# Optimization experiments

Hardware: AMD Instinct MI355X
Metric: run time of the kernel (lower is better)

The kernel has to match this reference:

```python
import jax, jax.numpy as jnp
import numpy as np

N = 1024
X_DIM = 256
Y_DIM = 256
HIDDEN = 256


def setup_inputs() -> dict:
    key = jax.random.key(0)
    ks = jax.random.split(key, 6)
    lim1 = 1.0 / np.sqrt(X_DIM + Y_DIM)
    lim2 = 1.0 / np.sqrt(HIDDEN)
    return {
        "x_samples": jax.random.normal(ks[0], (N, X_DIM), jnp.float32),
        "y_samples": jax.random.normal(ks[1], (N, Y_DIM), jnp.float32),
        # F_func params: Linear(x_dim+y_dim, hidden) -> ReLU -> Linear(hidden, 1)
        "W1": jax.random.uniform(ks[2], (X_DIM + Y_DIM, HIDDEN), jnp.float32, -lim1, lim1),
        "b1": jax.random.uniform(ks[3], (HIDDEN,), jnp.float32, -lim1, lim1),
        "W2": jax.random.uniform(ks[4], (HIDDEN, 1), jnp.float32, -lim2, lim2),
        "b2": jax.random.uniform(ks[5], (1,), jnp.float32, -lim2, lim2),
    }


def reference(x_samples, y_samples, W1, b1, W2, b2):
    n = y_samples.shape[0]
    # Diagonal (joint) term: F([x_i, y_i])
    t0 = jnp.maximum(jnp.concatenate([x_samples, y_samples], axis=-1) @ W1 + b1, 0.0) @ W2 + b2  # [N,1]
    # Pairwise term: decompose first Linear into x- and y-projections, broadcast-sum.
    px = x_samples @ W1[:X_DIM]   # [N, H]
    py = y_samples @ W1[X_DIM:]   # [N, H]
    # torch layout: row axis = y tile, col axis = x tile -> h[i, j] = relu(py_i + px_j + b1)
    h = jnp.maximum(py[:, None, :] + px[None, :, :] + b1, 0.0)          # [N, N, H]
    t1 = jnp.einsum("yxh,ho->yx", h, W2) + b2[0] - 1.0                   # [N, N]
    # logsumexp over dim=1 (x axis), then exp-mean
    lse = jax.nn.logsumexp(t1, axis=1) - jnp.log(jnp.float32(n))         # [N]
    lower_bound = t0.mean() - jnp.exp(lse).mean()
    return lower_bound
```

## Files before the change

### kernel.cpp

```cpp
#include <hip/hip_runtime.h>

#define NS 1024
#define KD 256
#define H  256
#define NBLK 256

__global__ __launch_bounds__(256) void proj_kernel(
    const float* __restrict__ X, const float* __restrict__ Y,
    const float* __restrict__ W1, const float* __restrict__ b1,
    float* __restrict__ PX, float* __restrict__ PYB, int* __restrict__ counter)
{
    if (blockIdx.x == 0 && blockIdx.y == 0 && blockIdx.z == 0 && threadIdx.x == 0)
        *counter = 0;

    const int z = blockIdx.z;
    const float* __restrict__ A = z ? Y : X;
    const float* __restrict__ W = W1 + (z ? KD * H : 0);
    float* __restrict__ OUT = z ? PYB : PX;

    __shared__ float xs[KD][34];

    const int tid = threadIdx.x;
    const int tx = tid & 15;
    const int ty = tid >> 4;
    const int i0 = blockIdx.y * 32, h0 = blockIdx.x * 64;

    {
        const int ii = tid & 31, q = tid >> 5;
        #pragma unroll
        for (int u = 0; u < 8; ++u) {
            const int k = u * 32 + q * 4;
            float4 v = *(const float4*)&A[(i0 + ii) * KD + k];
            xs[k + 0][ii] = v.x; xs[k + 1][ii] = v.y;
            xs[k + 2][ii] = v.z; xs[k + 3][ii] = v.w;
        }
    }
    __syncthreads();

    float acc[2][4] = {};
    const float* __restrict__ wp = &W[h0 + tx * 4];

    #pragma unroll 8
    for (int k = 0; k < KD; ++k) {
        float4 w4 = *(const float4*)&wp[k * H];
        const float x0 = xs[k][ty * 2 + 0];
        const float x1 = xs[k][ty * 2 + 1];
        acc[0][0] = fmaf(x0, w4.x, acc[0][0]);
        acc[0][1] = fmaf(x0, w4.y, acc[0][1]);
        acc[0][2] = fmaf(x0, w4.z, acc[0][2]);
        acc[0][3] = fmaf(x0, w4.w, acc[0][3]);
        acc[1][0] = fmaf(x1, w4.x, acc[1][0]);
        acc[1][1] = fmaf(x1, w4.y, acc[1][1]);
        acc[1][2] = fmaf(x1, w4.z, acc[1][2]);
        acc[1][3] = fmaf(x1, w4.w, acc[1][3]);
    }

    float bv[4] = {0.f, 0.f, 0.f, 0.f};
    if (z) *(float4*)bv = *(const float4*)&b1[h0 + tx * 4];
    #pragma unroll
    for (int r = 0; r < 2; ++r) {
        float o[4];
        #pragma unroll
        for (int c = 0; c < 4; ++c) o[c] = acc[r][c] + bv[c];
        *(float4*)&OUT[(i0 + ty * 2 + r) * H + h0 + tx * 4] = *(float4*)o;
    }
}

#define PXPAD 132
#define PYPAD 34

__global__ __launch_bounds__(256) void pair_kernel(
    const float* __restrict__ PX, const float* __restrict__ PYB,
    const float* __restrict__ W2, const float* __restrict__ b2,
    float* __restrict__ eparts, float* __restrict__ dparts,
    int* __restrict__ counter, float* __restrict__ out)
{
    __shared__ float pxt[2][64][PXPAD];
    __shared__ float pyt[2][64][PYPAD];
    __shared__ float red_e[256], red_d[256];
    __shared__ double sde[256], sdd[256];
    __shared__ int lastflag;

    const int tid = threadIdx.x;
    const int tx = tid & 15;
    const int ty = tid >> 4;
    const int j0 = blockIdx.x * 128, i0 = blockIdx.y * 32;

    const int su = tid & 7;
    const int sjb = tid >> 3;
    const int sii = tid & 31;
    const int sq = tid >> 5;

    float acc[2][8] = {};

#define STAGE(T, B)                                                                  \
    {                                                                                \
        const int hb = (T) * 64;                                                     \
        _Pragma("unroll")                                                            \
        for (int t = 0; t < 4; ++t) {                                                \
            _Pragma("unroll")                                                        \
            for (int s = 0; s < 2; ++s) {                                            \
                const int j = sjb + 32 * t;                                          \
                const int hh = (su + 8 * s) * 4;                                     \
                float4 v = *(const float4*)&PX[(j0 + j) * H + hb + hh];              \
                pxt[B][hh + 0][j] = v.x; pxt[B][hh + 1][j] = v.y;                    \
                pxt[B][hh + 2][j] = v.z; pxt[B][hh + 3][j] = v.w;                    \
            }                                                                        \
        }                                                                            \
        _Pragma("unroll")                                                            \
        for (int s = 0; s < 2; ++s) {                                                \
            const int hh = sq * 8 + s * 4;                                           \
            float4 v = *(const float4*)&PYB[(i0 + sii) * H + hb + hh];               \
            pyt[B][hh + 0][sii] = v.x; pyt[B][hh + 1][sii] = v.y;                    \
            pyt[B][hh + 2][sii] = v.z; pyt[B][hh + 3][sii] = v.w;                    \
        }                                                                            \
    }

    STAGE(0, 0);
    __syncthreads();

    for (int t = 0; t < 4; ++t) {
        const int cur = t & 1;
        if (t < 3) {
            if ((t & 1) == 0) STAGE(t + 1, 1)
            else              STAGE(t + 1, 0)
        }
        const int hb = t * 64;
        #pragma unroll 4
        for (int hh = 0; hh < 64; ++hh) {
            const float w = W2[hb + hh];
            const float py0 = pyt[cur][hh][ty * 2 + 0];
            const float py1 = pyt[cur][hh][ty * 2 + 1];
            float a4[4], b4[4];
            *(float4*)a4 = *(const float4*)&pxt[cur][hh][tx * 4];
            *(float4*)b4 = *(const float4*)&pxt[cur][hh][64 + tx * 4];
            #pragma unroll
            for (int c = 0; c < 4; ++c) {
                acc[0][c]     = fmaf(fmaxf(py0 + a4[c], 0.f), w, acc[0][c]);
                acc[1][c]     = fmaf(fmaxf(py1 + a4[c], 0.f), w, acc[1][c]);
                acc[0][4 + c] = fmaf(fmaxf(py0 + b4[c], 0.f), w, acc[0][4 + c]);
                acc[1][4 + c] = fmaf(fmaxf(py1 + b4[c], 0.f), w, acc[1][4 + c]);
            }
        }
        __syncthreads();
    }

    const float c0 = b2[0] - 1.0f;
    float esum = 0.f, dsum = 0.f;
    #pragma unroll
    for (int r = 0; r < 2; ++r) {
        const int irow = i0 + ty * 2 + r;
        #pragma unroll
        for (int g = 0; g < 2; ++g)
            #pragma unroll
            for (int c = 0; c < 4; ++c) {
                const float t1 = acc[r][g * 4 + c] + c0;
                esum += expf(t1);
                if (irow == j0 + g * 64 + tx * 4 + c) dsum += t1 + 1.0f;
            }
    }

    red_e[tid] = esum;
    red_d[tid] = dsum;
    __syncthreads();
    for (int s = 128; s > 0; s >>= 1) {
        if (tid < s) {
            red_e[tid] += red_e[tid + s];
            red_d[tid] += red_d[tid + s];
        }
        __syncthreads();
    }

    const int bid = blockIdx.y * gridDim.x + blockIdx.x;
    if (tid == 0) {
        __hip_atomic_store(&eparts[bid], red_e[0], __ATOMIC_RELAXED, __HIP_MEMORY_SCOPE_AGENT);
        __hip_atomic_store(&dparts[bid], red_d[0], __ATOMIC_RELAXED, __HIP_MEMORY_SCOPE_AGENT);
        __threadfence();
        const int prev = __hip_atomic_fetch_add(counter, 1, __ATOMIC_ACQ_REL, __HIP_MEMORY_SCOPE_AGENT);
        lastflag = (prev == NBLK - 1);
    }
    __syncthreads();

    if (lastflag) {
        __threadfence();
        sde[tid] = (double)__hip_atomic_load(&eparts[tid], __ATOMIC_RELAXED, __HIP_MEMORY_SCOPE_AGENT);
        sdd[tid] = (double)__hip_atomic_load(&dparts[tid], __ATOMIC_RELAXED, __HIP_MEMORY_SCOPE_AGENT);
        __syncthreads();
        for (int s = 128; s > 0; s >>= 1) {
            if (tid < s) { sde[tid] += sde[tid + s]; sdd[tid] += sdd[tid + s]; }
            __syncthreads();
        }
        if (tid == 0)
            out[0] = (float)(sdd[0] / (double)NS - sde[0] / ((double)NS * (double)NS));
    }
}

extern "C" void kernel_launch(void* const* d_in, const int* in_sizes, int n_in,
                              void* d_out, int out_size, void* d_ws, size_t ws_size,
                              hipStream_t stream)
{
    const float* X  = (const float*)d_in[0];
    const float* Y  = (const float*)d_in[1];
    const float* W1 = (const float*)d_in[2];
    const float* b1 = (const float*)d_in[3];
    const float* W2 = (const float*)d_in[4];
    const float* b2 = (const float*)d_in[5];
    float* out = (float*)d_out;

    float* PX     = (float*)d_ws;
    float* PYB    = PX + NS * H;
    float* eparts = PYB + NS * H;
    float* dparts = eparts + 256;
    int*   counter = (int*)(dparts + 256);

    proj_kernel<<<dim3(H / 64, NS / 32, 2), 256, 0, stream>>>(X, Y, W1, b1, PX, PYB, counter);
    pair_kernel<<<dim3(8, 32), 256, 0, stream>>>(PX, PYB, W2, b2, eparts, dparts, counter, out);
}
```

Baseline: 122.0 us.

## Fold W2 into projections and use relu(a)=(a+|a|)/2 with sign-partitioned hidden units

The projection kernel now scales each hidden unit by its W2 weight and permutes units so that positive-weight units come first. The pair kernel computes w*relu(s) as 0.5*(s + |s|) for positive w and 0.5*(s - |s|) for negative w. The linear parts factor into per-row and per-column sums, so the inner loop becomes an add plus an abs-accumulate with no multiply. The pair kernel also switches to square 64x64 tiles with a 4x4 register block, swizzled shared memory, and register-staged prefetch. The risks are the per-step sign branch and extra fp32 rounding from the reassociation.

New measurement: 125.5 us. 1.03x slower.

```diff
diff --git a/kernel.cpp b/kernel.cpp
--- a/kernel.cpp
+++ b/kernel.cpp
@@ -5,24 +5,47 @@
 #define H  256
 #define NBLK 256
 
+__device__ __forceinline__ int ldsw(int hh, int j) {
+    return (hh << 6) + ((j + ((hh >> 2) << 2)) & 63);
+}
+
 __global__ __launch_bounds__(256) void proj_kernel(
     const float* __restrict__ X, const float* __restrict__ Y,
     const float* __restrict__ W1, const float* __restrict__ b1,
-    float* __restrict__ PX, float* __restrict__ PYB, int* __restrict__ counter)
+    const float* __restrict__ W2,
+    float* __restrict__ PXW, float* __restrict__ PYW, int* __restrict__ counter)
 {
     if (blockIdx.x == 0 && blockIdx.y == 0 && blockIdx.z == 0 && threadIdx.x == 0)
         *counter = 0;
 
+    __shared__ float xs[KD][34];
+    __shared__ int dsts[H];
+    __shared__ int woff[4];
+
+    const int tid = threadIdx.x;
+
+    {
+        const float w = W2[tid];
+        const bool pos = (w >= 0.0f);
+        const unsigned long long m = __ballot(pos);
+        const int lane = tid & 63, wv = tid >> 6;
+        const int below = __popcll(m & ((1ull << lane) - 1ull));
+        if (lane == 0) woff[wv] = __popcll(m);
+        __syncthreads();
+        const int npos = woff[0] + woff[1] + woff[2] + woff[3];
+        int posbase = 0;
+        #pragma unroll
+        for (int q = 0; q < 4; ++q) if (q < wv) posbase += woff[q];
+        const int negbase = npos + (wv * 64 - posbase);
+        dsts[tid] = pos ? (posbase + below) : (negbase + (lane - below));
+    }
+
     const int z = blockIdx.z;
     const float* __restrict__ A = z ? Y : X;
     const float* __restrict__ W = W1 + (z ? KD * H : 0);
-    float* __restrict__ OUT = z ? PYB : PX;
-
-    __shared__ float xs[KD][34];
-
-    const int tid = threadIdx.x;
-    const int tx = tid & 15;
-    const int ty = tid >> 4;
+    float* __restrict__ OUT = z ? PYW : PXW;
+
+    const int tx = tid & 15, ty = tid >> 4;
     const int i0 = blockIdx.y * 32, h0 = blockIdx.x * 64;
 
     {
@@ -39,7 +62,6 @@
 
     float acc[2][4] = {};
     const float* __restrict__ wp = &W[h0 + tx * 4];
-
     #pragma unroll 8
     for (int k = 0; k < KD; ++k) {
         float4 w4 = *(const float4*)&wp[k * H];
@@ -57,108 +79,151 @@
 
     float bv[4] = {0.f, 0.f, 0.f, 0.f};
     if (z) *(float4*)bv = *(const float4*)&b1[h0 + tx * 4];
+    float wv4[4];
+    *(float4*)wv4 = *(const float4*)&W2[h0 + tx * 4];
+    int d4[4];
+    *(int4*)d4 = *(const int4*)&dsts[h0 + tx * 4];
+
     #pragma unroll
     for (int r = 0; r < 2; ++r) {
-        float o[4];
-        #pragma unroll
-        for (int c = 0; c < 4; ++c) o[c] = acc[r][c] + bv[c];
-        *(float4*)&OUT[(i0 + ty * 2 + r) * H + h0 + tx * 4] = *(float4*)o;
-    }
-}
-
-#define PXPAD 132
-#define PYPAD 34
+        const int row = i0 + ty * 2 + r;
+        #pragma unroll
+        for (int c = 0; c < 4; ++c)
+            OUT[row * H + d4[c]] = (acc[r][c] + bv[c]) * wv4[c];
+    }
+}
 
 __global__ __launch_bounds__(256) void pair_kernel(
-    const float* __restrict__ PX, const float* __restrict__ PYB,
+    const float* __restrict__ PXW, const float* __restrict__ PYW,
     const float* __restrict__ W2, const float* __restrict__ b2,
     float* __restrict__ eparts, float* __restrict__ dparts,
     int* __restrict__ counter, float* __restrict__ out)
 {
-    __shared__ float pxt[2][64][PXPAD];
-    __shared__ float pyt[2][64][PYPAD];
+    __shared__ float pxt[2][64 * 64];
+    __shared__ float pyt[2][64 * 64];
+    __shared__ float fpx[4 * 64], fpy[4 * 64];
     __shared__ float red_e[256], red_d[256];
     __shared__ double sde[256], sdd[256];
+    __shared__ int wcnt[4];
     __shared__ int lastflag;
 
     const int tid = threadIdx.x;
-    const int tx = tid & 15;
-    const int ty = tid >> 4;
-    const int j0 = blockIdx.x * 128, i0 = blockIdx.y * 32;
-
-    const int su = tid & 7;
-    const int sjb = tid >> 3;
-    const int sii = tid & 31;
-    const int sq = tid >> 5;
-
-    float acc[2][8] = {};
-
-#define STAGE(T, B)                                                                  \
-    {                                                                                \
-        const int hb = (T) * 64;                                                     \
-        _Pragma("unroll")                                                            \
-        for (int t = 0; t < 4; ++t) {                                                \
-            _Pragma("unroll")                                                        \
-            for (int s = 0; s < 2; ++s) {                                            \
-                const int j = sjb + 32 * t;                                          \
-                const int hh = (su + 8 * s) * 4;                                     \
-                float4 v = *(const float4*)&PX[(j0 + j) * H + hb + hh];              \
-                pxt[B][hh + 0][j] = v.x; pxt[B][hh + 1][j] = v.y;                    \
-                pxt[B][hh + 2][j] = v.z; pxt[B][hh + 3][j] = v.w;                    \
-            }                                                                        \
-        }                                                                            \
-        _Pragma("unroll")                                                            \
-        for (int s = 0; s < 2; ++s) {                                                \
-            const int hh = sq * 8 + s * 4;                                           \
-            float4 v = *(const float4*)&PYB[(i0 + sii) * H + hb + hh];               \
-            pyt[B][hh + 0][sii] = v.x; pyt[B][hh + 1][sii] = v.y;                    \
-            pyt[B][hh + 2][sii] = v.z; pyt[B][hh + 3][sii] = v.w;                    \
-        }                                                                            \
-    }
-
-    STAGE(0, 0);
-    __syncthreads();
-
-    for (int t = 0; t < 4; ++t) {
-        const int cur = t & 1;
-        if (t < 3) {
-            if ((t & 1) == 0) STAGE(t + 1, 1)
-            else              STAGE(t + 1, 0)
-        }
-        const int hb = t * 64;
-        #pragma unroll 4
-        for (int hh = 0; hh < 64; ++hh) {
-            const float w = W2[hb + hh];
-            const float py0 = pyt[cur][hh][ty * 2 + 0];
-            const float py1 = pyt[cur][hh][ty * 2 + 1];
-            float a4[4], b4[4];
-            *(float4*)a4 = *(const float4*)&pxt[cur][hh][tx * 4];
-            *(float4*)b4 = *(const float4*)&pxt[cur][hh][64 + tx * 4];
+    const int tx = tid & 15, ty = tid >> 4;
+    const int j0 = blockIdx.x * 64, i0 = blockIdx.y * 64;
+
+    {
+        const float w = W2[tid];
+        const unsigned long long m = __ballot(w >= 0.0f);
+        if ((tid & 63) == 0) wcnt[tid >> 6] = __popcll(m);
+    }
+
+    const int su = tid & 15, jb = tid >> 4;
+    float4 sx[4], sy[4];
+
+#define GLOAD(T)                                                              \
+    {                                                                         \
+        const int hb = (T) * 64;                                              \
+        _Pragma("unroll")                                                     \
+        for (int t = 0; t < 4; ++t) {                                         \
+            sx[t] = *(const float4*)&PXW[(j0 + jb + 16 * t) * H + hb + su * 4];\
+            sy[t] = *(const float4*)&PYW[(i0 + jb + 16 * t) * H + hb + su * 4];\
+        }                                                                     \
+    }
+
+#define SWRITE(B)                                                             \
+    {                                                                         \
+        _Pragma("unroll")                                                     \
+        for (int t = 0; t < 4; ++t) {                                         \
+            const int j = jb + 16 * t;                                        \
+            pxt[B][ldsw(su * 4 + 0, j)] = sx[t].x;                            \
+            pxt[B][ldsw(su * 4 + 1, j)] = sx[t].y;                            \
+            pxt[B][ldsw(su * 4 + 2, j)] = sx[t].z;                            \
+            pxt[B][ldsw(su * 4 + 3, j)] = sx[t].w;                            \
+            pyt[B][ldsw(su * 4 + 0, j)] = sy[t].x;                            \
+            pyt[B][ldsw(su * 4 + 1, j)] = sy[t].y;                            \
+            pyt[B][ldsw(su * 4 + 2, j)] = sy[t].z;                            \
+            pyt[B][ldsw(su * 4 + 3, j)] = sy[t].w;                            \
+        }                                                                     \
+    }
+
+    GLOAD(0);
+    SWRITE(0);
+    __syncthreads();
+    const int Npos = wcnt[0] + wcnt[1] + wcnt[2] + wcnt[3];
+
+    float accP[4][4] = {}, accN[4][4] = {};
+    float fx = 0.f, fy = 0.f;
+    const int fj = tid & 63, fq = tid >> 6;
+
+    for (int T = 0; T < 4; ++T) {
+        const int cur = T & 1;
+        if (T < 3) GLOAD(T + 1);
+        const int hb = T * 64;
+
+        #pragma unroll
+        for (int g = 0; g < 16; ++g) {
+            const int rot = (g << 2);
+            const float* bx = &pxt[cur][(g << 8) + ((tx * 4 + rot) & 63)];
+            const float* by = &pyt[cur][(g << 8) + ((ty * 4 + rot) & 63)];
             #pragma unroll
-            for (int c = 0; c < 4; ++c) {
-                acc[0][c]     = fmaf(fmaxf(py0 + a4[c], 0.f), w, acc[0][c]);
-                acc[1][c]     = fmaf(fmaxf(py1 + a4[c], 0.f), w, acc[1][c]);
-                acc[0][4 + c] = fmaf(fmaxf(py0 + b4[c], 0.f), w, acc[0][4 + c]);
-                acc[1][4 + c] = fmaf(fmaxf(py1 + b4[c], 0.f), w, acc[1][4 + c]);
+            for (int k = 0; k < 4; ++k) {
+                float px4[4], py4[4];
+                *(float4*)px4 = *(const float4*)&bx[k * 64];
+                *(float4*)py4 = *(const float4*)&by[k * 64];
+                if (hb + (g << 2) + k < Npos) {
+                    #pragma unroll
+                    for (int r = 0; r < 4; ++r)
+                        #pragma unroll
+                        for (int c = 0; c < 4; ++c)
+                            accP[r][c] += fabsf(py4[r] + px4[c]);
+                } else {
+                    #pragma unroll
+                    for (int r = 0; r < 4; ++r)
+                        #pragma unroll
+                        for (int c = 0; c < 4; ++c)
+                            accN[r][c] += fabsf(py4[r] + px4[c]);
+                }
             }
         }
-        __syncthreads();
-    }
+
+        #pragma unroll
+        for (int s = 0; s < 16; ++s) {
+            const int hh = fq * 16 + s;
+            fx += pxt[cur][ldsw(hh, fj)];
+            fy += pyt[cur][ldsw(hh, fj)];
+        }
+
+        if (T < 3) SWRITE((T + 1) & 1);
+        __syncthreads();
+    }
+
+    fpx[fq * 64 + fj] = fx;
+    fpy[fq * 64 + fj] = fy;
+    __syncthreads();
 
     const float c0 = b2[0] - 1.0f;
+    float ffe[4], gge[4];
+    #pragma unroll
+    for (int c = 0; c < 4; ++c) {
+        const int j = tx * 4 + c;
+        ffe[c] = 0.5f * (fpx[j] + fpx[64 + j] + fpx[128 + j] + fpx[192 + j]);
+    }
+    #pragma unroll
+    for (int r = 0; r < 4; ++r) {
+        const int i = ty * 4 + r;
+        gge[r] = 0.5f * (fpy[i] + fpy[64 + i] + fpy[128 + i] + fpy[192 + i]) + c0;
+    }
+
     float esum = 0.f, dsum = 0.f;
     #pragma unroll
-    for (int r = 0; r < 2; ++r) {
-        const int irow = i0 + ty * 2 + r;
-        #pragma unroll
-        for (int g = 0; g < 2; ++g)
-            #pragma unroll
-            for (int c = 0; c < 4; ++c) {
-                const float t1 = acc[r][g * 4 + c] + c0;
-                esum += expf(t1);
-                if (irow == j0 + g * 64 + tx * 4 + c) dsum += t1 + 1.0f;
-            }
-    }
+    for (int r = 0; r < 4; ++r)
+        #pragma unroll
+        for (int c = 0; c < 4; ++c) {
+            const float A = accP[r][c] - accN[r][c];
+            const float t1 = fmaf(0.5f, A, gge[r] + ffe[c]);
+            esum += expf(t1);
+            if (i0 + ty * 4 + r == j0 + tx * 4 + c) dsum += t1 + 1.0f;
+        }
 
     red_e[tid] = esum;
     red_d[tid] = dsum;
@@ -193,6 +258,8 @@
         if (tid == 0)
             out[0] = (float)(sdd[0] / (double)NS - sde[0] / ((double)NS * (double)NS));
     }
+#undef GLOAD
+#undef SWRITE
 }
 
 extern "C" void kernel_launch(void* const* d_in, const int* in_sizes, int n_in,
@@ -207,12 +274,12 @@
     const float* b2 = (const float*)d_in[5];
     float* out = (float*)d_out;
 
-    float* PX     = (float*)d_ws;
-    float* PYB    = PX + NS * H;
-    float* eparts = PYB + NS * H;
+    float* PXW    = (float*)d_ws;
+    float* PYW    = PXW + NS * H;
+    float* eparts = PYW + NS * H;
     float* dparts = eparts + 256;
     int*   counter = (int*)(dparts + 256);
 
-    proj_kernel<<<dim3(H / 64, NS / 32, 2), 256, 0, stream>>>(X, Y, W1, b1, PX, PYB, counter);
-    pair_kernel<<<dim3(8, 32), 256, 0, stream>>>(PX, PYB, W2, b2, eparts, dparts, counter, out);
-}
+    proj_kernel<<<dim3(4, 32, 2), 256, 0, stream>>>(X, Y, W1, b1, W2, PXW, PYW, counter);
+    pair_kernel<<<dim3(16, 16), 256, 0, stream>>>(PXW, PYW, W2, b2, eparts, dparts, counter, out);
+}
```

## Use relu(a)=(a+|a|)/2 identity to move linear terms out of pair loop

Applied to the files above, without the earlier changes.

Rewrites relu(py+px) as half of (py+px)+|py+px|, so the linear part collapses into per-row and per-column dot products with W2 (FX, GY), computed in the projection kernel via atomics. The pair loop then does only add, abs and FMA per element. Projections are stored transposed (h-major) so px tiles can be staged with direct global-to-LDS loads, and py values are read straight from global memory. The pair grid is retiled to 16x128 with 512 blocks, and a memset clears the accumulators and counter. The changes are reassociation of float sums and extra atomics in the projection stage.

New measurement: 142.8 us. +17.1%, slower.

```diff
diff --git a/kernel.cpp b/kernel.cpp
--- a/kernel.cpp
+++ b/kernel.cpp
@@ -3,27 +3,33 @@
 #define NS 1024
 #define KD 256
 #define H  256
-#define NBLK 256
+#define PAIR_NBLK 512
+
+#define GLOAD_LDS16(gp, lp)                                                         \
+    __builtin_amdgcn_global_load_lds(                                               \
+        (const __attribute__((address_space(1))) void*)(gp),                        \
+        (__attribute__((address_space(3))) void*)(lp), 16, 0, 0)
 
 __global__ __launch_bounds__(256) void proj_kernel(
     const float* __restrict__ X, const float* __restrict__ Y,
     const float* __restrict__ W1, const float* __restrict__ b1,
-    float* __restrict__ PX, float* __restrict__ PYB, int* __restrict__ counter)
+    const float* __restrict__ W2,
+    float* __restrict__ PXT, float* __restrict__ PYT,
+    float* __restrict__ FX, float* __restrict__ GY)
 {
-    if (blockIdx.x == 0 && blockIdx.y == 0 && blockIdx.z == 0 && threadIdx.x == 0)
-        *counter = 0;
-
     const int z = blockIdx.z;
     const float* __restrict__ A = z ? Y : X;
-    const float* __restrict__ W = W1 + (z ? KD * H : 0);
-    float* __restrict__ OUT = z ? PYB : PX;
+    const float* __restrict__ W = W1 + (z ? (size_t)KD * H : 0);
+    float* __restrict__ OUT = z ? PYT : PXT;
+    float* __restrict__ RS  = z ? GY : FX;
 
     __shared__ float xs[KD][34];
+    __shared__ float fred[8][33];
 
     const int tid = threadIdx.x;
-    const int tx = tid & 15;
-    const int ty = tid >> 4;
-    const int i0 = blockIdx.y * 32, h0 = blockIdx.x * 64;
+    const int jl = tid & 31;
+    const int hg = tid >> 5;
+    const int i0 = blockIdx.y * 32, h0 = blockIdx.x * 32;
 
     {
         const int ii = tid & 31, q = tid >> 5;
@@ -37,127 +43,117 @@
     }
     __syncthreads();
 
-    float acc[2][4] = {};
-    const float* __restrict__ wp = &W[h0 + tx * 4];
-
+    float acc[4] = {};
+    const float* __restrict__ wp = &W[h0 + hg * 4];
     #pragma unroll 8
     for (int k = 0; k < KD; ++k) {
-        float4 w4 = *(const float4*)&wp[k * H];
-        const float x0 = xs[k][ty * 2 + 0];
-        const float x1 = xs[k][ty * 2 + 1];
-        acc[0][0] = fmaf(x0, w4.x, acc[0][0]);
-        acc[0][1] = fmaf(x0, w4.y, acc[0][1]);
-        acc[0][2] = fmaf(x0, w4.z, acc[0][2]);
-        acc[0][3] = fmaf(x0, w4.w, acc[0][3]);
-        acc[1][0] = fmaf(x1, w4.x, acc[1][0]);
-        acc[1][1] = fmaf(x1, w4.y, acc[1][1]);
-        acc[1][2] = fmaf(x1, w4.z, acc[1][2]);
-        acc[1][3] = fmaf(x1, w4.w, acc[1][3]);
-    }
-
-    float bv[4] = {0.f, 0.f, 0.f, 0.f};
-    if (z) *(float4*)bv = *(const float4*)&b1[h0 + tx * 4];
+        float4 w4 = *(const float4*)&wp[(size_t)k * H];
+        const float xv = xs[k][jl];
+        acc[0] = fmaf(xv, w4.x, acc[0]);
+        acc[1] = fmaf(xv, w4.y, acc[1]);
+        acc[2] = fmaf(xv, w4.z, acc[2]);
+        acc[3] = fmaf(xv, w4.w, acc[3]);
+    }
+
+    if (z) {
+        float4 bv = *(const float4*)&b1[h0 + hg * 4];
+        acc[0] += bv.x; acc[1] += bv.y; acc[2] += bv.z; acc[3] += bv.w;
+    }
+
+    float4 w2v = *(const float4*)&W2[h0 + hg * 4];
+    float fp = 0.f;
+    const float w2a[4] = {w2v.x, w2v.y, w2v.z, w2v.w};
     #pragma unroll
-    for (int r = 0; r < 2; ++r) {
-        float o[4];
-        #pragma unroll
-        for (int c = 0; c < 4; ++c) o[c] = acc[r][c] + bv[c];
-        *(float4*)&OUT[(i0 + ty * 2 + r) * H + h0 + tx * 4] = *(float4*)o;
+    for (int c = 0; c < 4; ++c) {
+        const int h = h0 + hg * 4 + c;
+        OUT[(size_t)h * NS + i0 + jl] = acc[c];
+        fp = fmaf(w2a[c], acc[c], fp);
+    }
+    fred[hg][jl] = fp;
+    __syncthreads();
+    if (tid < 32) {
+        float s = 0.f;
+        #pragma unroll
+        for (int g = 0; g < 8; ++g) s += fred[g][tid];
+        atomicAdd(&RS[i0 + tid], s);
     }
 }
 
-#define PXPAD 132
-#define PYPAD 34
-
 __global__ __launch_bounds__(256) void pair_kernel(
-    const float* __restrict__ PX, const float* __restrict__ PYB,
+    const float* __restrict__ PXT, const float* __restrict__ PYT,
     const float* __restrict__ W2, const float* __restrict__ b2,
+    const float* __restrict__ FX, const float* __restrict__ GY,
     float* __restrict__ eparts, float* __restrict__ dparts,
     int* __restrict__ counter, float* __restrict__ out)
 {
-    __shared__ float pxt[2][64][PXPAD];
-    __shared__ float pyt[2][64][PYPAD];
+    __shared__ float pxs[2][32][128];
     __shared__ float red_e[256], red_d[256];
     __shared__ double sde[256], sdd[256];
     __shared__ int lastflag;
 
     const int tid = threadIdx.x;
-    const int tx = tid & 15;
-    const int ty = tid >> 4;
-    const int j0 = blockIdx.x * 128, i0 = blockIdx.y * 32;
-
-    const int su = tid & 7;
-    const int sjb = tid >> 3;
-    const int sii = tid & 31;
-    const int sq = tid >> 5;
-
-    float acc[2][8] = {};
-
-#define STAGE(T, B)                                                                  \
-    {                                                                                \
-        const int hb = (T) * 64;                                                     \
-        _Pragma("unroll")                                                            \
-        for (int t = 0; t < 4; ++t) {                                                \
-            _Pragma("unroll")                                                        \
-            for (int s = 0; s < 2; ++s) {                                            \
-                const int j = sjb + 32 * t;                                          \
-                const int hh = (su + 8 * s) * 4;                                     \
-                float4 v = *(const float4*)&PX[(j0 + j) * H + hb + hh];              \
-                pxt[B][hh + 0][j] = v.x; pxt[B][hh + 1][j] = v.y;                    \
-                pxt[B][hh + 2][j] = v.z; pxt[B][hh + 3][j] = v.w;                    \
-            }                                                                        \
-        }                                                                            \
-        _Pragma("unroll")                                                            \
-        for (int s = 0; s < 2; ++s) {                                                \
-            const int hh = sq * 8 + s * 4;                                           \
-            float4 v = *(const float4*)&PYB[(i0 + sii) * H + hb + hh];               \
-            pyt[B][hh + 0][sii] = v.x; pyt[B][hh + 1][sii] = v.y;                    \
-            pyt[B][hh + 2][sii] = v.z; pyt[B][hh + 3][sii] = v.w;                    \
-        }                                                                            \
+    const int lane = tid & 63;
+    const int wid = __builtin_amdgcn_readfirstlane(tid >> 6);
+    const int j0 = blockIdx.x * 128;
+    const int i0 = blockIdx.y * 16;
+
+#define STAGE(T, B)                                                             \
+    {                                                                           \
+        const float* gb = &PXT[(size_t)((T) * 32) * NS + j0];                   \
+        _Pragma("unroll")                                                       \
+        for (int p = 0; p < 4; ++p) {                                           \
+            const int hrow = 8 * p + 2 * wid + (lane >> 5);                     \
+            const float* g = gb + (size_t)hrow * NS + (lane & 31) * 4;          \
+            float* l = &pxs[B][hrow][(lane & 31) * 4];                          \
+            GLOAD_LDS16(g, l);                                                  \
+        }                                                                       \
     }
 
     STAGE(0, 0);
     __syncthreads();
 
-    for (int t = 0; t < 4; ++t) {
-        const int cur = t & 1;
-        if (t < 3) {
-            if ((t & 1) == 0) STAGE(t + 1, 1)
-            else              STAGE(t + 1, 0)
-        }
-        const int hb = t * 64;
-        #pragma unroll 4
-        for (int hh = 0; hh < 64; ++hh) {
-            const float w = W2[hb + hh];
-            const float py0 = pyt[cur][hh][ty * 2 + 0];
-            const float py1 = pyt[cur][hh][ty * 2 + 1];
-            float a4[4], b4[4];
-            *(float4*)a4 = *(const float4*)&pxt[cur][hh][tx * 4];
-            *(float4*)b4 = *(const float4*)&pxt[cur][hh][64 + tx * 4];
+    float acc[4][2] = {};
+    const float* __restrict__ pyb = &PYT[i0 + wid * 4];
+
+    for (int T = 0; T < 8; ++T) {
+        const int B = T & 1;
+        if (T < 7) STAGE(T + 1, B ^ 1);
+        #pragma unroll
+        for (int g = 0; g < 8; ++g) {
+            float4 w4 = *(const float4*)&W2[T * 32 + g * 4];
+            const float wa[4] = {w4.x, w4.y, w4.z, w4.w};
             #pragma unroll
-            for (int c = 0; c < 4; ++c) {
-                acc[0][c]     = fmaf(fmaxf(py0 + a4[c], 0.f), w, acc[0][c]);
-                acc[1][c]     = fmaf(fmaxf(py1 + a4[c], 0.f), w, acc[1][c]);
-                acc[0][4 + c] = fmaf(fmaxf(py0 + b4[c], 0.f), w, acc[0][4 + c]);
-                acc[1][4 + c] = fmaf(fmaxf(py1 + b4[c], 0.f), w, acc[1][4 + c]);
+            for (int k = 0; k < 4; ++k) {
+                const int hh = g * 4 + k;
+                float2 px2 = *(const float2*)&pxs[B][hh][lane * 2];
+                float4 p4 = *(const float4*)&pyb[(size_t)(T * 32 + hh) * NS];
+                const float pya[4] = {p4.x, p4.y, p4.z, p4.w};
+                #pragma unroll
+                for (int r = 0; r < 4; ++r) {
+                    acc[r][0] = fmaf(fabsf(pya[r] + px2.x), wa[k], acc[r][0]);
+                    acc[r][1] = fmaf(fabsf(pya[r] + px2.y), wa[k], acc[r][1]);
+                }
             }
         }
         __syncthreads();
     }
 
     const float c0 = b2[0] - 1.0f;
+    float2 fx2 = *(const float2*)&FX[j0 + lane * 2];
+    float4 g4 = *(const float4*)&GY[i0 + wid * 4];
+    const float gya[4] = {g4.x, g4.y, g4.z, g4.w};
+    const float fxa[2] = {fx2.x, fx2.y};
+
     float esum = 0.f, dsum = 0.f;
     #pragma unroll
-    for (int r = 0; r < 2; ++r) {
-        const int irow = i0 + ty * 2 + r;
-        #pragma unroll
-        for (int g = 0; g < 2; ++g)
-            #pragma unroll
-            for (int c = 0; c < 4; ++c) {
-                const float t1 = acc[r][g * 4 + c] + c0;
-                esum += expf(t1);
-                if (irow == j0 + g * 64 + tx * 4 + c) dsum += t1 + 1.0f;
-            }
+    for (int r = 0; r < 4; ++r) {
+        const int irow = i0 + wid * 4 + r;
+        #pragma unroll
+        for (int c = 0; c < 2; ++c) {
+            const float t1 = fmaf(0.5f, acc[r][c] + gya[r] + fxa[c], c0);
+            esum += expf(t1);
+            if (irow == j0 + lane * 2 + c) dsum += t1 + 1.0f;
+        }
     }
 
     red_e[tid] = esum;
@@ -177,14 +173,16 @@
         __hip_atomic_store(&dparts[bid], red_d[0], __ATOMIC_RELAXED, __HIP_MEMORY_SCOPE_AGENT);
         __threadfence();
         const int prev = __hip_atomic_fetch_add(counter, 1, __ATOMIC_ACQ_REL, __HIP_MEMORY_SCOPE_AGENT);
-        lastflag = (prev == NBLK - 1);
+        lastflag = (prev == PAIR_NBLK - 1);
     }
     __syncthreads();
 
     if (lastflag) {
         __threadfence();
-        sde[tid] = (double)__hip_atomic_load(&eparts[tid], __ATOMIC_RELAXED, __HIP_MEMORY_SCOPE_AGENT);
-        sdd[tid] = (double)__hip_atomic_load(&dparts[tid], __ATOMIC_RELAXED, __HIP_MEMORY_SCOPE_AGENT);
+        sde[tid] = (double)__hip_atomic_load(&eparts[tid], __ATOMIC_RELAXED, __HIP_MEMORY_SCOPE_AGENT)
+                 + (double)__hip_atomic_load(&eparts[tid + 256], __ATOMIC_RELAXED, __HIP_MEMORY_SCOPE_AGENT);
+        sdd[tid] = (double)__hip_atomic_load(&dparts[tid], __ATOMIC_RELAXED, __HIP_MEMORY_SCOPE_AGENT)
+                 + (double)__hip_atomic_load(&dparts[tid + 256], __ATOMIC_RELAXED, __HIP_MEMORY_SCOPE_AGENT);
         __syncthreads();
         for (int s = 128; s > 0; s >>= 1) {
             if (tid < s) { sde[tid] += sde[tid + s]; sdd[tid] += sdd[tid + s]; }
@@ -193,6 +191,7 @@
         if (tid == 0)
             out[0] = (float)(sdd[0] / (double)NS - sde[0] / ((double)NS * (double)NS));
     }
+#undef STAGE
 }
 
 extern "C" void kernel_launch(void* const* d_in, const int* in_sizes, int n_in,
@@ -207,12 +206,17 @@
     const float* b2 = (const float*)d_in[5];
     float* out = (float*)d_out;
 
-    float* PX     = (float*)d_ws;
-    float* PYB    = PX + NS * H;
-    float* eparts = PYB + NS * H;
-    float* dparts = eparts + 256;
-    int*   counter = (int*)(dparts + 256);
-
-    proj_kernel<<<dim3(H / 64, NS / 32, 2), 256, 0, stream>>>(X, Y, W1, b1, PX, PYB, counter);
-    pair_kernel<<<dim3(8, 32), 256, 0, stream>>>(PX, PYB, W2, b2, eparts, dparts, counter, out);
+    float* PXT    = (float*)d_ws;
+    float* PYT    = PXT + (size_t)H * NS;
+    float* eparts = PYT + (size_t)H * NS;
+    float* dparts = eparts + 512;
+    float* FX     = dparts + 512;
+    float* GY     = FX + NS;
+    int*   counter = (int*)(GY + NS);
+
+    hipMemsetAsync(FX, 0, (size_t)(2 * NS) * sizeof(float) + sizeof(int), stream);
+
+    proj_kernel<<<dim3(8, 32, 2), 256, 0, stream>>>(X, Y, W1, b1, W2, PXT, PYT, FX, GY);
+    pair_kernel<<<dim3(8, 64), 256, 0, stream>>>(PXT, PYT, W2, b2, FX, GY,
+                                                 eparts, dparts, counter, out);
 }
```
